# Kernel optimization log

Measured on AMD Instinct MI355X. Metric: run time of the kernel, lower is better.

Reference implementation:

```python
import jax, jax.numpy as jnp
import numpy as np

B, Q, P, K, E, H = 2, 2500, 2500, 2500, 256, 8
D = E // H
FF = 2 * E
EPS = 1e-5


def layernorm(x, g, b):
    mu = jnp.mean(x, axis=-1, keepdims=True)
    var = jnp.var(x, axis=-1, keepdims=True)
    return (x - mu) * jax.lax.rsqrt(var + EPS) * g + b


def mha(q_in, k_in, v_in, wq, wk, wv, scale):
    n, ql = q_in.shape[0], q_in.shape[1]
    q = (q_in @ wq).reshape(n, ql, H, D)
    k = (k_in @ wk).reshape(n, k_in.shape[1], H, D)
    v = (v_in @ wv).reshape(n, v_in.shape[1], H, D)
    scores = jnp.einsum('nqhd,nkhd->nhqk', q, k) / scale
    attn = jax.nn.softmax(scores, axis=-1)
    return jnp.einsum('nhqk,nkhd->nqhd', attn, v).reshape(n, ql, E)


def setup_inputs() -> dict:
    key = jax.random.key(0)
    ks = jax.random.split(key, 24)
    s = lambda i, shape, sc=0.02: jax.random.normal(ks[i], shape, dtype=jnp.float32) * sc
    return {
        'prev_seq': jax.random.normal(ks[0], (B, P, E), dtype=jnp.float32),
        'query': jax.random.normal(ks[1], (B, Q, E), dtype=jnp.float32),
        'img_ft': jax.random.normal(ks[2], (B, K, E), dtype=jnp.float32),
        't_wq': s(3, (E, E)), 't_wk': s(4, (E, E)), 't_wv': s(5, (E, E)),
        's_wq': s(6, (E, E)), 's_wk': s(7, (E, E)), 's_wv': s(8, (E, E)),
        's_wo': s(9, (E, E)), 's_bo': jnp.zeros((E,), jnp.float32),
        'n1_g': jnp.ones((E,), jnp.float32), 'n1_b': jnp.zeros((E,), jnp.float32),
        'n2_g': jnp.ones((E,), jnp.float32), 'n2_b': jnp.zeros((E,), jnp.float32),
        'n3_g': jnp.ones((E,), jnp.float32), 'n3_b': jnp.zeros((E,), jnp.float32),
        'ff_w1': s(10, (E, FF)), 'ff_b1': jnp.zeros((FF,), jnp.float32),
        'ff_w2': s(11, (FF, E)), 'ff_b2': jnp.zeros((E,), jnp.float32),
    }


def reference(prev_seq, query, img_ft, t_wq, t_wk, t_wv, s_wq, s_wk, s_wv,
              s_wo, s_bo, n1_g, n1_b, n2_g, n2_b, n3_g, n3_b,
              ff_w1, ff_b1, ff_w2, ff_b2):
    # Temporal self-attention: K/V from prev_seq, scale = sqrt(embed_size)
    attn = mha(query, prev_seq, prev_seq, t_wq, t_wk, t_wv, float(E) ** 0.5)
    x = layernorm(attn + query, n1_g, n1_b)
    # Spatial cross-attention: K/V from img_ft, scale = sqrt(head_dim), with fc_out
    cross = mha(x, img_ft, img_ft, s_wq, s_wk, s_wv, float(D) ** 0.5)
    cross = cross @ s_wo + s_bo
    x = layernorm(cross + x, n2_g, n2_b)
    # FFN: E -> 2E -> ReLU -> E
    ff = jax.nn.relu(x @ ff_w1 + ff_b1) @ ff_w2 + ff_b2
    return layernorm(ff + x, n3_g, n3_b)
```

## Files before the change

kernel.cpp:

```cpp
#include <hip/hip_runtime.h>
#include <hip/hip_bf16.h>
#include <stdint.h>


typedef __bf16 bf16_t;
typedef __bf16 bf16x8 __attribute__((ext_vector_type(8)));
typedef __bf16 bf16x4 __attribute__((ext_vector_type(4)));
typedef float  f32x4  __attribute__((ext_vector_type(4)));
typedef float  f32x16 __attribute__((ext_vector_type(16)));
typedef uint32_t u32;
typedef uint32_t u32x4 __attribute__((ext_vector_type(4)));

#define NB   2
#define SEQ  2500
#define EMB  256
#define NH   8
#define HD   32
#define MTOT (NB*SEQ)
#define KVSPLIT 3
#define SPLITLEN 834
#define NPAIR 14

static __device__ __forceinline__ f32x4 mfma16(bf16x8 a, bf16x8 b, f32x4 c) {
  return __builtin_amdgcn_mfma_f32_16x16x32_bf16(a, b, c, 0, 0, 0);
}
static __device__ __forceinline__ f32x16 mfma32(bf16x8 a, bf16x8 b, f32x16 c) {
  return __builtin_amdgcn_mfma_f32_32x32x16_bf16(a, b, c, 0, 0, 0);
}
static __device__ __forceinline__ u32 pack2(float a, float b) {
  union { __bf16 h; unsigned short s; } x, y;
  x.h = (__bf16)a; y.h = (__bf16)b;
  return (u32)x.s | ((u32)y.s << 16);
}

__global__ __launch_bounds__(256) void prep_kernel(
    const float* s0, const float* s1, const float* s2, const float* s3,
    const float* s4, const float* s5, const float* s6, const float* s7,
    const float* s8, bf16_t* wt,
    const float* aq, const float* ap, const float* ai,
    bf16_t* dq, bf16_t* dp, bf16_t* di)
{
  int b = blockIdx.x;
  if (b < 176) {
    const float* src; int R, C, tl; size_t doff;
    if (b < 112) {
      int mi = b >> 4; tl = b & 15; R = 256; C = 256; doff = (size_t)mi * 65536;
      switch (mi) {
        case 0: src = s0; break; case 1: src = s1; break; case 2: src = s2; break;
        case 3: src = s3; break; case 4: src = s4; break; case 5: src = s5; break;
        default: src = s6;
      }
    } else if (b < 144) { tl = b - 112; R = 256; C = 512; doff = 458752; src = s7; }
    else                { tl = b - 144; R = 512; C = 256; doff = 589824; src = s8; }
    const int tpr = C >> 6;
    const int tr = tl / tpr, tc = tl % tpr;
    bf16_t* dst = wt + doff;
    #pragma unroll
    for (int i = 0; i < 16; ++i) {
      int lin = i * 256 + threadIdx.x;
      int lr = lin >> 6, lc = lin & 63;
      int rr = tr * 64 + lr, cc = tc * 64 + lc;
      dst[(size_t)cc * R + rr] = (__bf16)src[(size_t)rr * C + cc];
    }
    return;
  }
  int idx = b - 176;
  int t = idx / 313, r = idx % 313;
  const float* src = (t == 0) ? aq : (t == 1) ? ap : ai;
  bf16_t* dst = (t == 0) ? dq : (t == 1) ? dp : di;
  #pragma unroll
  for (int k = 0; k < 4; ++k) {
    int i = r * 1024 + k * 256 + threadIdx.x;
    if (i < 320000) {
      float4 v = ((const float4*)src)[i];
      bf16x4 o;
      o[0] = (__bf16)v.x; o[1] = (__bf16)v.y; o[2] = (__bf16)v.z; o[3] = (__bf16)v.w;
      ((bf16x4*)dst)[i] = o;
    }
  }
}

template<int K>
static __device__ __forceinline__ void gemm32_body(
    const bf16_t* __restrict__ A, const bf16_t* __restrict__ Wt,
    const float* __restrict__ bias, bf16_t* __restrict__ Cout,
    int M, int N, int relu, float cscale, int bx, int by)
{
  const int tid = threadIdx.x;
  const int lane = tid & 63, wid = tid >> 6;
  const int l31 = lane & 31, hi = lane >> 5;
  const int mbase = bx * 128 + wid * 32;
  const int nbase = by * 64;

  int arow = mbase + l31; if (arow > M - 1) arow = M - 1;
  const bf16_t* ap = A + (size_t)arow * K + hi * 8;
  const bf16_t* bp = Wt + (size_t)(nbase + l31) * K + hi * 8;

  f32x16 acc0 = {}, acc1 = {};
  #pragma unroll
  for (int kk = 0; kk < K; kk += 16) {
    bf16x8 a  = *(const bf16x8*)(ap + kk);
    bf16x8 b0 = *(const bf16x8*)(bp + kk);
    bf16x8 b1 = *(const bf16x8*)(bp + (size_t)32 * K + kk);
    acc0 = mfma32(a, b0, acc0);
    acc1 = mfma32(a, b1, acc1);
  }
  #pragma unroll
  for (int r = 0; r < 16; ++r) {
    const int row = mbase + (r & 3) + ((r >> 2) << 3) + hi * 4;
    if (row < M) {
      const int c0 = nbase + l31;
      const int c1 = nbase + 32 + l31;
      float v0 = acc0[r] * cscale + (bias ? bias[c0] : 0.f);
      float v1 = acc1[r] * cscale + (bias ? bias[c1] : 0.f);
      if (relu) { v0 = fmaxf(v0, 0.f); v1 = fmaxf(v1, 0.f); }
      Cout[(size_t)row * N + c0] = (bf16_t)v0;
      Cout[(size_t)row * N + c1] = (bf16_t)v1;
    }
  }
}

__global__ __launch_bounds__(256) void gemm_relu_kernel(
    const bf16_t* __restrict__ A, const bf16_t* __restrict__ Wt,
    const float* __restrict__ bias, bf16_t* __restrict__ Cout,
    int M, int N)
{
  gemm32_body<256>(A, Wt, bias, Cout, M, N, 1, 1.f, blockIdx.x, blockIdx.y);
}

__global__ __launch_bounds__(256) void proj5_kernel(
    const bf16_t* qbf, const bf16_t* pbf, const bf16_t* ibf,
    const bf16_t* WT,
    bf16_t* tq, bf16_t* tk, bf16_t* tv, bf16_t* sk, bf16_t* sv, float qsc)
{
  const int z = blockIdx.z;
  const bf16_t* A; const bf16_t* W; bf16_t* C; float cs = 1.f;
  switch (z) {
    case 0:  A = qbf; W = WT;          C = tq; cs = qsc; break;
    case 1:  A = pbf; W = WT + 65536;  C = tk; break;
    case 2:  A = pbf; W = WT + 131072; C = tv; break;
    case 3:  A = ibf; W = WT + 262144; C = sk; break;
    default: A = ibf; W = WT + 327680; C = sv; break;
  }
  gemm32_body<256>(A, W, nullptr, C, MTOT, 256, 0, cs, blockIdx.x, blockIdx.y);
}

__global__ __launch_bounds__(256) void projq_kernel(
    const bf16_t* __restrict__ A, const bf16_t* __restrict__ W,
    bf16_t* __restrict__ C, float sc)
{
  gemm32_body<256>(A, W, nullptr, C, MTOT, 256, 0, sc, blockIdx.x, blockIdx.y);
}

__global__ __launch_bounds__(256) void gemm_ln_merge_kernel(
    const bf16_t* __restrict__ Op0, const bf16_t* __restrict__ Op1,
    const bf16_t* __restrict__ Op2, const float* __restrict__ Lp,
    const bf16_t* __restrict__ Wt, const float* __restrict__ bias,
    const bf16_t* __restrict__ resid, const float* __restrict__ gw,
    const float* __restrict__ bw, bf16_t* __restrict__ OutB, int M)
{
  __shared__ float red[16][4][2];
  const int tid = threadIdx.x;
  const int lane = tid & 63, wid = tid >> 6;
  const int l15 = lane & 15, g = lane >> 4;
  const int mbase = blockIdx.x * 16;
  const int nbase = wid * 64;

  int arow = mbase + l15; if (arow > M - 1) arow = M - 1;
  const int b = arow / SEQ, q = arow - b * SEQ;

  float invLh[8];
  #pragma unroll
  for (int h = 0; h < 8; ++h) {
    const size_t lb = (size_t)(b * 8 + h) * SEQ + q;
    invLh[h] = 1.f / (Lp[lb] + Lp[lb + (size_t)16 * SEQ]
                              + Lp[lb + (size_t)32 * SEQ]);
  }
  const size_t ob0 = ((size_t)(b * 8) * SEQ + q) * 32 + g * 8;
  const bf16_t* bp = Wt + (size_t)(nbase + l15) * 256 + g * 8;

  f32x4 acc[4];
  #pragma unroll
  for (int j = 0; j < 4; ++j) acc[j] = (f32x4){0.f,0.f,0.f,0.f};

  #pragma unroll
  for (int kk = 0; kk < 256; kk += 32) {
    const int h = kk >> 5;
    const size_t ob = ob0 + (size_t)h * (SEQ * 32);
    bf16x8 o0 = *(const bf16x8*)(Op0 + ob);
    bf16x8 o1 = *(const bf16x8*)(Op1 + ob);
    bf16x8 o2 = *(const bf16x8*)(Op2 + ob);
    const float inv = invLh[h];
    bf16x8 a;
    #pragma unroll
    for (int j = 0; j < 8; ++j)
      a[j] = (__bf16)(((float)o0[j] + (float)o1[j] + (float)o2[j]) * inv);
    #pragma unroll
    for (int ct = 0; ct < 4; ++ct) {
      bf16x8 bfr = *(const bf16x8*)(bp + (size_t)ct * 16 * 256 + kk);
      acc[ct] = mfma16(a, bfr, acc[ct]);
    }
  }

  float x[4][4];
  float xs[4] = {0.f,0.f,0.f,0.f}, xq[4] = {0.f,0.f,0.f,0.f};
  #pragma unroll
  for (int ct = 0; ct < 4; ++ct) {
    const int col = nbase + ct * 16 + l15;
    const float bv = bias[col];
    #pragma unroll
    for (int r = 0; r < 4; ++r) {
      int row = mbase + g * 4 + r; if (row > M - 1) row = M - 1;
      float v = acc[ct][r] + bv + (float)resid[(size_t)row * EMB + col];
      x[ct][r] = v;
      xs[r] += v; xq[r] += v * v;
    }
  }
  #pragma unroll
  for (int r = 0; r < 4; ++r) {
    #pragma unroll
    for (int m = 1; m < 16; m <<= 1) {
      xs[r] += __shfl_xor(xs[r], m);
      xq[r] += __shfl_xor(xq[r], m);
    }
  }
  if (l15 == 0) {
    #pragma unroll
    for (int r = 0; r < 4; ++r) {
      red[g * 4 + r][wid][0] = xs[r];
      red[g * 4 + r][wid][1] = xq[r];
    }
  }
  __syncthreads();
  #pragma unroll
  for (int r = 0; r < 4; ++r) {
    const int rl = g * 4 + r;
    const float S = red[rl][0][0] + red[rl][1][0] + red[rl][2][0] + red[rl][3][0];
    const float Q = red[rl][0][1] + red[rl][1][1] + red[rl][2][1] + red[rl][3][1];
    const float mean = S * (1.f / EMB);
    const float var = Q * (1.f / EMB) - mean * mean;
    const float rstd = rsqrtf(var + 1e-5f);
    const int row = mbase + rl;
    if (row < M) {
      #pragma unroll
      for (int ct = 0; ct < 4; ++ct) {
        const int col = nbase + ct * 16 + l15;
        OutB[(size_t)row * EMB + col] =
            (bf16_t)((x[ct][r] - mean) * rstd * gw[col] + bw[col]);
      }
    }
  }
}

template<int K>
__global__ __launch_bounds__(256) void gemm_ln_kernel(
    const bf16_t* __restrict__ A, const bf16_t* __restrict__ Wt,
    const float* __restrict__ bias, const bf16_t* __restrict__ resid,
    const float* __restrict__ gw, const float* __restrict__ bw,
    bf16_t* __restrict__ OutB, float* __restrict__ OutF, int M)
{
  __shared__ float red[16][4][2];
  const int tid = threadIdx.x;
  const int lane = tid & 63, wid = tid >> 6;
  const int l15 = lane & 15, g = lane >> 4;
  const int mbase = blockIdx.x * 16;
  const int nbase = wid * 64;

  int arow = mbase + l15; if (arow > M - 1) arow = M - 1;
  const bf16_t* ap = A + (size_t)arow * K + g * 8;
  const bf16_t* bp = Wt + (size_t)(nbase + l15) * K + g * 8;

  f32x4 acc[4];
  #pragma unroll
  for (int j = 0; j < 4; ++j) acc[j] = (f32x4){0.f,0.f,0.f,0.f};

  #pragma unroll
  for (int kk = 0; kk < K; kk += 32) {
    bf16x8 a = *(const bf16x8*)(ap + kk);
    #pragma unroll
    for (int ct = 0; ct < 4; ++ct) {
      bf16x8 bfr = *(const bf16x8*)(bp + (size_t)ct * 16 * K + kk);
      acc[ct] = mfma16(a, bfr, acc[ct]);
    }
  }

  float x[4][4];
  float xs[4] = {0.f,0.f,0.f,0.f}, xq[4] = {0.f,0.f,0.f,0.f};
  #pragma unroll
  for (int ct = 0; ct < 4; ++ct) {
    const int col = nbase + ct * 16 + l15;
    const float bv = bias[col];
    #pragma unroll
    for (int r = 0; r < 4; ++r) {
      int row = mbase + g * 4 + r; if (row > M - 1) row = M - 1;
      float v = acc[ct][r] + bv + (float)resid[(size_t)row * EMB + col];
      x[ct][r] = v;
      xs[r] += v; xq[r] += v * v;
    }
  }
  #pragma unroll
  for (int r = 0; r < 4; ++r) {
    #pragma unroll
    for (int m = 1; m < 16; m <<= 1) {
      xs[r] += __shfl_xor(xs[r], m);
      xq[r] += __shfl_xor(xq[r], m);
    }
  }
  if (l15 == 0) {
    #pragma unroll
    for (int r = 0; r < 4; ++r) {
      red[g * 4 + r][wid][0] = xs[r];
      red[g * 4 + r][wid][1] = xq[r];
    }
  }
  __syncthreads();
  #pragma unroll
  for (int r = 0; r < 4; ++r) {
    const int rl = g * 4 + r;
    const float S = red[rl][0][0] + red[rl][1][0] + red[rl][2][0] + red[rl][3][0];
    const float Q = red[rl][0][1] + red[rl][1][1] + red[rl][2][1] + red[rl][3][1];
    const float mean = S * (1.f / EMB);
    const float var = Q * (1.f / EMB) - mean * mean;
    const float rstd = rsqrtf(var + 1e-5f);
    const int row = mbase + rl;
    if (row < M) {
      #pragma unroll
      for (int ct = 0; ct < 4; ++ct) {
        const int col = nbase + ct * 16 + l15;
        const float y = (x[ct][r] - mean) * rstd * gw[col] + bw[col];
        if (OutF) OutF[(size_t)row * EMB + col] = y;
        else      OutB[(size_t)row * EMB + col] = (bf16_t)y;
      }
    }
  }
}

__global__ __launch_bounds__(256, 2) void attn_part_kernel(
    const bf16_t* __restrict__ Qm, const bf16_t* __restrict__ Km,
    const bf16_t* __restrict__ Vm, bf16_t* __restrict__ Op0,
    bf16_t* __restrict__ Op1, bf16_t* __restrict__ Op2,
    float* __restrict__ Lp)
{
  __shared__ bf16_t Vt[4][32][40];

  const int tid = threadIdx.x;
  const int lane = tid & 63, wid = tid >> 6;
  const int q32 = lane & 31, hi = lane >> 5;

  const int n = blockIdx.x;
  const int vid = (n & 7) * 60 + (n >> 3);
  const int grp = vid / 10;
  const int sub = vid - grp * 10;
  const int bh = grp / 3;
  const int split = grp - bh * 3;

  const size_t qoff = (size_t)(bh >> 3) * SEQ * EMB + (bh & 7) * HD;
  const int kv_begin = split * SPLITLEN;
  const int kv_end = min(kv_begin + SPLITLEN, SEQ);

  const int qbase = sub * 256 + wid * 64;
  const int qrX = min(qbase + q32, SEQ - 1);
  const int qrY = min(qbase + 32 + q32, SEQ - 1);
  const bf16x8 qfaX = *(const bf16x8*)(Qm + qoff + (size_t)qrX * EMB + hi * 8);
  const bf16x8 qfbX = *(const bf16x8*)(Qm + qoff + (size_t)qrX * EMB + 16 + hi * 8);
  const bf16x8 qfaY = *(const bf16x8*)(Qm + qoff + (size_t)qrY * EMB + hi * 8);
  const bf16x8 qfbY = *(const bf16x8*)(Qm + qoff + (size_t)qrY * EMB + 16 + hi * 8);

  f32x16 accAX = {}, accBX = {}, accAY = {}, accBY = {};
  float lsumX = 0.f, lsumY = 0.f;

  const int skv = tid >> 3;
  const int sd0 = (tid & 7) << 2;
  const int scc = (skv + ((sd0 >> 3) << 3)) & 31;

  const bf16_t* kp = Km + qoff + (size_t)(kv_begin + q32) * EMB + hi * 8;
  const bf16_t* vp = Vm + qoff + (size_t)(kv_begin + skv) * EMB + sd0;

  bf16x4 vA = *(const bf16x4*)vp;
  bf16x4 vB = *(const bf16x4*)(vp + 32 * EMB);
  bf16x8 kaA = *(const bf16x8*)kp;
  bf16x8 kbA = *(const bf16x8*)(kp + 16);
  bf16x8 kaB = *(const bf16x8*)(kp + 32 * EMB);
  bf16x8 kbB = *(const bf16x8*)(kp + 32 * EMB + 16);
  kp += 64 * EMB;
  vp += 64 * EMB;

#define TREE16(dst, p)                                                         \
    {                                                                          \
      float t0 = p[0] + p[1],  t1 = p[2] + p[3];                               \
      float t2 = p[4] + p[5],  t3 = p[6] + p[7];                               \
      float t4 = p[8] + p[9],  t5 = p[10] + p[11];                             \
      float t6 = p[12] + p[13], t7 = p[14] + p[15];                            \
      float u0 = t0 + t1, u1 = t2 + t3, u2 = t4 + t5, u3 = t6 + t7;            \
      dst = (u0 + u1) + (u2 + u3);                                             \
    }

#define SOFTPACK(p, f1, f2)                                                    \
    {                                                                          \
      u32 w0 = pack2(p[0], p[1]),   w1 = pack2(p[2], p[3]);                    \
      u32 w2 = pack2(p[4], p[5]),   w3 = pack2(p[6], p[7]);                    \
      u32 w4 = pack2(p[8], p[9]),   w5 = pack2(p[10], p[11]);                  \
      u32 w6 = pack2(p[12], p[13]), w7 = pack2(p[14], p[15]);                  \
      asm("v_permlane32_swap_b32 %0, %1" : "+v"(w0), "+v"(w2));                \
      asm("v_permlane32_swap_b32 %0, %1" : "+v"(w1), "+v"(w3));                \
      asm("v_permlane32_swap_b32 %0, %1" : "+v"(w4), "+v"(w6));                \
      asm("v_permlane32_swap_b32 %0, %1" : "+v"(w5), "+v"(w7));                \
      f1.x = w0; f1.y = w1; f1.z = w2; f1.w = w3;                              \
      f2.x = w4; f2.y = w5; f2.z = w6; f2.w = w7;                              \
    }

#define EXPALL(p, s) _Pragma("unroll")                                         \
    for (int r = 0; r < 16; ++r) p[r] = __builtin_amdgcn_exp2f(s[r]);

#define MASKT(p, kv0)                                                          \
    {                                                                          \
      _Pragma("unroll")                                                        \
      for (int r = 0; r < 16; ++r) {                                           \
        const int kvg = (kv0) + (r & 3) + ((r >> 2) << 3) + hi * 4;            \
        if (kvg >= kv_end) p[r] = 0.f;                                         \
      }                                                                        \
    }

#define ATTN_PAIR(P, MASKED, PREFETCH)                                         \
  {                                                                            \
    const int bufA = ((P) & 1) << 1, bufB = bufA + 1;                          \
    _Pragma("unroll")                                                          \
    for (int j = 0; j < 4; ++j) {                                              \
      Vt[bufA][sd0 + j][scc] = vA[j];                                          \
      Vt[bufB][sd0 + j][scc] = vB[j];                                          \
    }                                                                          \
    bf16x4 vAn, vBn; bf16x8 kaAn, kbAn, kaBn, kbBn;                            \
    if (PREFETCH) {                                                            \
      vAn = *(const bf16x4*)vp;                                                \
      vBn = *(const bf16x4*)(vp + 32 * EMB);                                   \
      kaAn = *(const bf16x8*)kp;                                               \
      kbAn = *(const bf16x8*)(kp + 16);                                        \
      kaBn = *(const bf16x8*)(kp + 32 * EMB);                                  \
      kbBn = *(const bf16x8*)(kp + 32 * EMB + 16);                             \
      kp += 64 * EMB; vp += 64 * EMB;                                          \
    }                                                                          \
    f32x16 sAX = {}, sBX = {}, sAY = {}, sBY = {};                             \
    sAX = mfma32(kaA, qfaX, sAX);                                              \
    sBX = mfma32(kaB, qfaX, sBX);                                              \
    sAY = mfma32(kaA, qfaY, sAY);                                              \
    sBY = mfma32(kaB, qfaY, sBY);                                              \
    sAX = mfma32(kbA, qfbX, sAX);                                              \
    sBX = mfma32(kbB, qfbX, sBX);                                              \
    sAY = mfma32(kbA, qfbY, sAY);                                              \
    sBY = mfma32(kbB, qfbY, sBY);                                              \
    float pAX[16], pBX[16], pAY[16], pBY[16];                                  \
    EXPALL(pAX, sAX) EXPALL(pBX, sBX) EXPALL(pAY, sAY) EXPALL(pBY, sBY)        \
    if (MASKED) {                                                              \
      const int kvA = kv_begin + (((P) << 1) << 5);                            \
      const int kvB = kvA + 32;                                                \
      MASKT(pAX, kvA) MASKT(pAY, kvA) MASKT(pBX, kvB) MASKT(pBY, kvB)          \
    }                                                                          \
    float ps0, ps1, ps2, ps3;                                                  \
    TREE16(ps0, pAX) TREE16(ps1, pBX) TREE16(ps2, pAY) TREE16(ps3, pBY)        \
    lsumX += ps0 + ps1; lsumY += ps2 + ps3;                                    \
    u32x4 f1AX, f2AX, f1BX, f2BX, f1AY, f2AY, f1BY, f2BY;                      \
    SOFTPACK(pAX, f1AX, f2AX)                                                  \
    SOFTPACK(pBX, f1BX, f2BX)                                                  \
    SOFTPACK(pAY, f1AY, f2AY)                                                  \
    SOFTPACK(pBY, f1BY, f2BY)                                                  \
    __syncthreads();                                                           \
    const int c1 = ((hi + (q32 >> 3)) & 3) << 3;                               \
    const int c2 = ((2 + hi + (q32 >> 3)) & 3) << 3;                           \
    bf16x8 vf1A = *(const bf16x8*)&Vt[bufA][q32][c1];                          \
    bf16x8 vf2A = *(const bf16x8*)&Vt[bufA][q32][c2];                          \
    bf16x8 vf1B = *(const bf16x8*)&Vt[bufB][q32][c1];                          \
    bf16x8 vf2B = *(const bf16x8*)&Vt[bufB][q32][c2];                          \
    accAX = mfma32(*(bf16x8*)&f1AX, vf1A, accAX);                              \
    accBX = mfma32(*(bf16x8*)&f1BX, vf1B, accBX);                              \
    accAY = mfma32(*(bf16x8*)&f1AY, vf1A, accAY);                              \
    accBY = mfma32(*(bf16x8*)&f1BY, vf1B, accBY);                              \
    accAX = mfma32(*(bf16x8*)&f2AX, vf2A, accAX);                              \
    accBX = mfma32(*(bf16x8*)&f2BX, vf2B, accBX);                              \
    accAY = mfma32(*(bf16x8*)&f2AY, vf2A, accAY);                              \
    accBY = mfma32(*(bf16x8*)&f2BY, vf2B, accBY);                              \
    if (PREFETCH) {                                                            \
      kaA = kaAn; kbA = kbAn; kaB = kaBn; kbB = kbBn;                          \
      vA = vAn; vB = vBn;                                                      \
    }                                                                          \
  }

  #pragma unroll
  for (int P = 0; P < NPAIR - 1; ++P) ATTN_PAIR(P, 0, 1)
  ATTN_PAIR(NPAIR - 1, 1, 0)
#undef ATTN_PAIR
#undef SOFTPACK
#undef TREE16
#undef EXPALL
#undef MASKT

  lsumX += __shfl_xor(lsumX, 32);
  lsumY += __shfl_xor(lsumY, 32);
  bf16_t* Opx = (split == 0) ? Op0 : (split == 1) ? Op1 : Op2;
  const size_t obase = (size_t)bh * SEQ;
  const size_t lbase = ((size_t)split * 16 + bh) * SEQ;
  #pragma unroll
  for (int r = 0; r < 16; ++r) {
    const int qX = qbase + (r & 3) + ((r >> 2) << 3) + hi * 4;
    const int qY = qX + 32;
    if (qX < SEQ) Opx[(obase + qX) * 32 + q32] = (bf16_t)(accAX[r] + accBX[r]);
    if (qY < SEQ) Opx[(obase + qY) * 32 + q32] = (bf16_t)(accAY[r] + accBY[r]);
  }
  if (lane < 32) {
    const int qX = qbase + lane, qY = qX + 32;
    if (qX < SEQ) Lp[lbase + qX] = lsumX;
    if (qY < SEQ) Lp[lbase + qY] = lsumY;
  }
}

__global__ __launch_bounds__(256) void merge_kernel(
    const bf16_t* __restrict__ Op0, const bf16_t* __restrict__ Op1,
    const bf16_t* __restrict__ Op2, const float* __restrict__ Lp,
    const bf16_t* __restrict__ resid, const float* __restrict__ gw,
    const float* __restrict__ bw, bf16_t* __restrict__ out)
{
  const int lane = threadIdx.x & 63, wid = threadIdx.x >> 6;
  const int row = blockIdx.x * 4 + wid;
  const int b = row / SEQ, q = row - b * SEQ;
  const int h = lane >> 3, dl = (lane & 7) * 4;
  const int bh = b * 8 + h;

  const size_t lb = (size_t)bh * SEQ + q;
  const float L = Lp[lb] + Lp[lb + (size_t)16 * SEQ] + Lp[lb + (size_t)32 * SEQ];
  const float invL = 1.f / L;

  const size_t pb = ((size_t)bh * SEQ + q) * 32 + dl;
  bf16x4 o0 = *(const bf16x4*)(Op0 + pb);
  bf16x4 o1 = *(const bf16x4*)(Op1 + pb);
  bf16x4 o2 = *(const bf16x4*)(Op2 + pb);

  const size_t base = (size_t)row * EMB + lane * 4;
  bf16x4 rv = *(const bf16x4*)(resid + base);
  float x[4], s = 0.f, sq = 0.f;
  #pragma unroll
  for (int j = 0; j < 4; ++j) {
    x[j] = ((float)o0[j] + (float)o1[j] + (float)o2[j]) * invL + (float)rv[j];
    s += x[j]; sq += x[j] * x[j];
  }
  #pragma unroll
  for (int m = 1; m < 64; m <<= 1) { s += __shfl_xor(s, m); sq += __shfl_xor(sq, m); }
  const float mean = s * (1.f / EMB);
  const float var = sq * (1.f / EMB) - mean * mean;
  const float rstd = rsqrtf(var + 1e-5f);
  float4 gv = *(const float4*)(gw + lane * 4);
  float4 bv = *(const float4*)(bw + lane * 4);
  bf16x4 ov;
  ov[0] = (__bf16)((x[0] - mean) * rstd * gv.x + bv.x);
  ov[1] = (__bf16)((x[1] - mean) * rstd * gv.y + bv.y);
  ov[2] = (__bf16)((x[2] - mean) * rstd * gv.z + bv.z);
  ov[3] = (__bf16)((x[3] - mean) * rstd * gv.w + bv.w);
  *(bf16x4*)(out + base) = ov;
}

extern "C" void kernel_launch(void* const* d_in, const int* in_sizes, int n_in,
                              void* d_out, int out_size, void* d_ws, size_t ws_size,
                              hipStream_t stream)
{
  (void)in_sizes; (void)n_in; (void)out_size; (void)ws_size;
  const float* prev  = (const float*)d_in[0];
  const float* query = (const float*)d_in[1];
  const float* img   = (const float*)d_in[2];
  const float* t_wq  = (const float*)d_in[3];
  const float* t_wk  = (const float*)d_in[4];
  const float* t_wv  = (const float*)d_in[5];
  const float* s_wq  = (const float*)d_in[6];
  const float* s_wk  = (const float*)d_in[7];
  const float* s_wv  = (const float*)d_in[8];
  const float* s_wo  = (const float*)d_in[9];
  const float* s_bo  = (const float*)d_in[10];
  const float* n1g = (const float*)d_in[11];
  const float* n1b = (const float*)d_in[12];
  const float* n2g = (const float*)d_in[13];
  const float* n2b = (const float*)d_in[14];
  const float* n3g = (const float*)d_in[15];
  const float* n3b = (const float*)d_in[16];
  const float* ffw1 = (const float*)d_in[17];
  const float* ffb1 = (const float*)d_in[18];
  const float* ffw2 = (const float*)d_in[19];
  const float* ffb2 = (const float*)d_in[20];

  bf16_t* ws   = (bf16_t*)d_ws;
  bf16_t* WT   = ws;
  bf16_t* WTF1 = ws + 458752;
  bf16_t* WTF2 = ws + 589824;
  bf16_t* qbf = ws + 720896;
  bf16_t* pbf = qbf + 1280000;
  bf16_t* ibf = pbf + 1280000;
  bf16_t* qb = ibf + 1280000;
  bf16_t* kb = qb + 1280000;
  bf16_t* vb = kb + 1280000;
  bf16_t* ab = vb + 1280000;
  bf16_t* x1 = ab + 1280000;
  bf16_t* cb = x1 + 1280000;
  bf16_t* x2r = cb + 1280000;
  bf16_t* hb = x2r + 1280000;
  bf16_t* fb = hb + 2560000;
  float* outp = (float*)d_out;

  bf16_t* Op0 = ab;
  bf16_t* Op1 = cb;
  bf16_t* Op2 = x2r;
  bf16_t* kb2 = hb;
  bf16_t* vb2 = hb + 1280000;
  bf16_t* X2 = vb;
  float*  Lp = (float*)pbf;

  const float log2e = 1.4426950408889634f;
  const float qscT = log2e * (1.f / 16.f);
  const float qscS = log2e * 0.17677669529663687f;

  dim3 blk(256);
  prep_kernel<<<1115, blk, 0, stream>>>(t_wq, t_wk, t_wv, s_wq, s_wk, s_wv,
                                        s_wo, ffw1, ffw2, ws,
                                        query, prev, img, qbf, pbf, ibf);

  dim3 gP5(40, 4, 5), gP1(40, 4), gG512(40, 8);
  proj5_kernel<<<gP5, blk, 0, stream>>>(qbf, pbf, ibf, WT,
                                        qb, kb, vb, kb2, vb2, qscT);
  attn_part_kernel<<<480, blk, 0, stream>>>(qb, kb, vb, Op0, Op1, Op2, Lp);
  merge_kernel<<<1250, blk, 0, stream>>>(Op0, Op1, Op2, Lp, qbf, n1g, n1b, x1);
  projq_kernel<<<gP1, blk, 0, stream>>>(x1, WT + 196608, qb, qscS);
  attn_part_kernel<<<480, blk, 0, stream>>>(qb, kb2, vb2, Op0, Op1, Op2, Lp);
  gemm_ln_merge_kernel<<<313, blk, 0, stream>>>(Op0, Op1, Op2, Lp,
                                                WT + 393216, s_bo, x1,
                                                n2g, n2b, X2, MTOT);
  gemm_relu_kernel<<<gG512, blk, 0, stream>>>(X2, WTF1, ffb1, hb, MTOT, 512);
  gemm_ln_kernel<512><<<313, blk, 0, stream>>>(hb, WTF2, ffb2, X2,
                                               n3g, n3b, nullptr, outp, MTOT);
  (void)fb;
}
```

Measured before the change: 165.7 us.

## Load V fragments directly from global memory, dropping LDS transpose and barrier

Removes the shared-memory V transpose buffer and its per-iteration __syncthreads. Instead, each lane gathers its transposed V fragment with strided scalar global loads, prefetched one pair ahead. It also regroups the exp/mask/sum/pack work into per-tile chains to shorten register live ranges. The cost is many more, narrower global loads, with each wave fetching the same V rows redundantly.

```diff
diff --git a/kernel.cpp b/kernel.cpp
--- a/kernel.cpp
+++ b/kernel.cpp
@@ -341,8 +341,6 @@
     bf16_t* __restrict__ Op1, bf16_t* __restrict__ Op2,
     float* __restrict__ Lp)
 {
-  __shared__ bf16_t Vt[4][32][40];
-
   const int tid = threadIdx.x;
   const int lane = tid & 63, wid = tid >> 6;
   const int q32 = lane & 31, hi = lane >> 5;
@@ -369,20 +367,26 @@
   f32x16 accAX = {}, accBX = {}, accAY = {}, accBY = {};
   float lsumX = 0.f, lsumY = 0.f;
 
-  const int skv = tid >> 3;
-  const int sd0 = (tid & 7) << 2;
-  const int scc = (skv + ((sd0 >> 3) << 3)) & 31;
-
   const bf16_t* kp = Km + qoff + (size_t)(kv_begin + q32) * EMB + hi * 8;
-  const bf16_t* vp = Vm + qoff + (size_t)(kv_begin + skv) * EMB + sd0;
-
-  bf16x4 vA = *(const bf16x4*)vp;
-  bf16x4 vB = *(const bf16x4*)(vp + 32 * EMB);
+  const bf16_t* vp = Vm + qoff + (size_t)kv_begin * EMB + q32 + (size_t)hi * 8 * EMB;
+
+#define LOADV(f1, f2, base)                                                    \
+    {                                                                          \
+      _Pragma("unroll")                                                        \
+      for (int e = 0; e < 8; ++e) {                                            \
+        f1[e] = (base)[(size_t)e * EMB];                                       \
+        f2[e] = (base)[(size_t)(16 + e) * EMB];                                \
+      }                                                                        \
+    }
+
   bf16x8 kaA = *(const bf16x8*)kp;
   bf16x8 kbA = *(const bf16x8*)(kp + 16);
   bf16x8 kaB = *(const bf16x8*)(kp + 32 * EMB);
   bf16x8 kbB = *(const bf16x8*)(kp + 32 * EMB + 16);
   kp += 64 * EMB;
+  bf16x8 vf1A, vf2A, vf1B, vf2B;
+  LOADV(vf1A, vf2A, vp)
+  LOADV(vf1B, vf2B, vp + 32 * EMB)
   vp += 64 * EMB;
 
 #define TREE16(dst, p)                                                         \
@@ -409,35 +413,37 @@
       f2.x = w4; f2.y = w5; f2.z = w6; f2.w = w7;                              \
     }
 
-#define EXPALL(p, s) _Pragma("unroll")                                         \
-    for (int r = 0; r < 16; ++r) p[r] = __builtin_amdgcn_exp2f(s[r]);
-
-#define MASKT(p, kv0)                                                          \
+#define CHAIN(s, MASKED, kv0, lsum, f1, f2)                                    \
     {                                                                          \
+      float p[16];                                                             \
       _Pragma("unroll")                                                        \
-      for (int r = 0; r < 16; ++r) {                                           \
-        const int kvg = (kv0) + (r & 3) + ((r >> 2) << 3) + hi * 4;            \
-        if (kvg >= kv_end) p[r] = 0.f;                                         \
+      for (int r = 0; r < 16; ++r) p[r] = __builtin_amdgcn_exp2f(s[r]);        \
+      if (MASKED) {                                                            \
+        _Pragma("unroll")                                                      \
+        for (int r = 0; r < 16; ++r) {                                         \
+          const int kvg = (kv0) + (r & 3) + ((r >> 2) << 3) + hi * 4;          \
+          if (kvg >= kv_end) p[r] = 0.f;                                       \
+        }                                                                      \
       }                                                                        \
+      float ps;                                                                \
+      TREE16(ps, p)                                                            \
+      lsum += ps;                                                              \
+      SOFTPACK(p, f1, f2)                                                      \
     }
 
 #define ATTN_PAIR(P, MASKED, PREFETCH)                                         \
   {                                                                            \
-    const int bufA = ((P) & 1) << 1, bufB = bufA + 1;                          \
-    _Pragma("unroll")                                                          \
-    for (int j = 0; j < 4; ++j) {                                              \
-      Vt[bufA][sd0 + j][scc] = vA[j];                                          \
-      Vt[bufB][sd0 + j][scc] = vB[j];                                          \
-    }                                                                          \
-    bf16x4 vAn, vBn; bf16x8 kaAn, kbAn, kaBn, kbBn;                            \
+    bf16x8 kaAn, kbAn, kaBn, kbBn;                                             \
+    bf16x8 vf1An, vf2An, vf1Bn, vf2Bn;                                         \
     if (PREFETCH) {                                                            \
-      vAn = *(const bf16x4*)vp;                                                \
-      vBn = *(const bf16x4*)(vp + 32 * EMB);                                   \
       kaAn = *(const bf16x8*)kp;                                               \
       kbAn = *(const bf16x8*)(kp + 16);                                        \
       kaBn = *(const bf16x8*)(kp + 32 * EMB);                                  \
       kbBn = *(const bf16x8*)(kp + 32 * EMB + 16);                             \
-      kp += 64 * EMB; vp += 64 * EMB;                                          \
+      kp += 64 * EMB;                                                          \
+      LOADV(vf1An, vf2An, vp)                                                  \
+      LOADV(vf1Bn, vf2Bn, vp + 32 * EMB)                                       \
+      vp += 64 * EMB;                                                          \
     }                                                                          \
     f32x16 sAX = {}, sBX = {}, sAY = {}, sBY = {};                             \
     sAX = mfma32(kaA, qfaX, sAX);                                              \
@@ -448,28 +454,13 @@
     sBX = mfma32(kbB, qfbX, sBX);                                              \
     sAY = mfma32(kbA, qfbY, sAY);                                              \
     sBY = mfma32(kbB, qfbY, sBY);                                              \
-    float pAX[16], pBX[16], pAY[16], pBY[16];                                  \
-    EXPALL(pAX, sAX) EXPALL(pBX, sBX) EXPALL(pAY, sAY) EXPALL(pBY, sBY)        \
-    if (MASKED) {                                                              \
-      const int kvA = kv_begin + (((P) << 1) << 5);                            \
-      const int kvB = kvA + 32;                                                \
-      MASKT(pAX, kvA) MASKT(pAY, kvA) MASKT(pBX, kvB) MASKT(pBY, kvB)          \
-    }                                                                          \
-    float ps0, ps1, ps2, ps3;                                                  \
-    TREE16(ps0, pAX) TREE16(ps1, pBX) TREE16(ps2, pAY) TREE16(ps3, pBY)        \
-    lsumX += ps0 + ps1; lsumY += ps2 + ps3;                                    \
+    const int kvA = kv_begin + (((P) << 1) << 5);                              \
+    const int kvB = kvA + 32;                                                  \
     u32x4 f1AX, f2AX, f1BX, f2BX, f1AY, f2AY, f1BY, f2BY;                      \
-    SOFTPACK(pAX, f1AX, f2AX)                                                  \
-    SOFTPACK(pBX, f1BX, f2BX)                                                  \
-    SOFTPACK(pAY, f1AY, f2AY)                                                  \
-    SOFTPACK(pBY, f1BY, f2BY)                                                  \
-    __syncthreads();                                                           \
-    const int c1 = ((hi + (q32 >> 3)) & 3) << 3;                               \
-    const int c2 = ((2 + hi + (q32 >> 3)) & 3) << 3;                           \
-    bf16x8 vf1A = *(const bf16x8*)&Vt[bufA][q32][c1];                          \
-    bf16x8 vf2A = *(const bf16x8*)&Vt[bufA][q32][c2];                          \
-    bf16x8 vf1B = *(const bf16x8*)&Vt[bufB][q32][c1];                          \
-    bf16x8 vf2B = *(const bf16x8*)&Vt[bufB][q32][c2];                          \
+    CHAIN(sAX, MASKED, kvA, lsumX, f1AX, f2AX)                                 \
+    CHAIN(sBX, MASKED, kvB, lsumX, f1BX, f2BX)                                 \
+    CHAIN(sAY, MASKED, kvA, lsumY, f1AY, f2AY)                                 \
+    CHAIN(sBY, MASKED, kvB, lsumY, f1BY, f2BY)                                 \
     accAX = mfma32(*(bf16x8*)&f1AX, vf1A, accAX);                              \
     accBX = mfma32(*(bf16x8*)&f1BX, vf1B, accBX);                              \
     accAY = mfma32(*(bf16x8*)&f1AY, vf1A, accAY);                              \
@@ -480,7 +471,7 @@
     accBY = mfma32(*(bf16x8*)&f2BY, vf2B, accBY);                              \
     if (PREFETCH) {                                                            \
       kaA = kaAn; kbA = kbAn; kaB = kaBn; kbB = kbBn;                          \
-      vA = vAn; vB = vBn;                                                      \
+      vf1A = vf1An; vf2A = vf2An; vf1B = vf1Bn; vf2B = vf2Bn;                  \
     }                                                                          \
   }
 
@@ -488,10 +479,10 @@
   for (int P = 0; P < NPAIR - 1; ++P) ATTN_PAIR(P, 0, 1)
   ATTN_PAIR(NPAIR - 1, 1, 0)
 #undef ATTN_PAIR
+#undef CHAIN
 #undef SOFTPACK
 #undef TREE16
-#undef EXPALL
-#undef MASKT
+#undef LOADV
 
   lsumX += __shfl_xor(lsumX, 32);
   lsumY += __shfl_xor(lsumY, 32);
```

New measurement: 171.1 us. 3.3% more time.
